# Optimization experiments

Measured on AMD Instinct MI355X. Metric: run time of the kernel, lower is better.

Reference implementation:

```python
import jax, jax.numpy as jnp
from jax import lax
import numpy as np

P = 16          # patch_len
EPS = 1e-5      # BatchNorm eps


def _dct_mats(L):
    # torch_dct DCT-II: ortho matrix Co and scale d s.t. dct(norm=None)(x) = (x @ Co.T) * d,
    # dct(norm='ortho')(x) = x @ Co.T, idct(norm=None)(y) = (y / d) @ Co
    n = jnp.arange(L, dtype=jnp.float32)
    base = jnp.cos(jnp.pi * (2.0 * n[None, :] + 1.0) * n[:, None] / (2.0 * L))
    ck = jnp.where(n == 0, 1.0 / jnp.sqrt(jnp.float32(L)), jnp.sqrt(2.0 / L))
    Co = base * ck[:, None]
    d = jnp.where(n == 0, 2.0 * jnp.sqrt(jnp.float32(L)), jnp.sqrt(2.0 * L))
    return Co, d


def _gelu(t):
    return jax.nn.gelu(t, approximate=False)  # torch nn.GELU default (erf)


def _dw(t, w, pad):  # depthwise Conv1d, t [B,D,L], w [D,k], SAME-style padding
    return lax.conv_general_dilated(t, w[:, None, :], (1,), [(pad, pad)],
                                    feature_group_count=t.shape[1],
                                    dimension_numbers=('NCH', 'OIH', 'NCH'))


def _forward(x, conv1_w, conv1_b, conv2_w, conv2_b, conv3_w, conv3_b,
             dn_g, dn_b, dn_m, dn_v, pn_g, pn_b, pn_m, pn_v,
             embed_w, embed_b, lin_res_w, lin_res_b,
             depth_res_w, depth_res_b, depth_conv_w, depth_conv_b,
             threshold, att_dw_w, att_dw_b, att_conv_w, att_conv_b,
             att_g, att_b, att_m, att_v, fc1_w, fc1_b, fc2_w, fc2_b):
    B, L, D = x.shape
    N = L // P                       # patch_num (stride == patch_len)
    Co, dvec = _dct_mats(L)

    conv1 = lambda t: t * conv1_w[:, None] + conv1_b[:, None]   # grouped 1x1 Conv1d
    bnD = lambda t: (t - dn_m[:, None]) * (dn_g[:, None] / jnp.sqrt(dn_v[:, None] + EPS)) + dn_b[:, None]

    xt = jnp.transpose(x, (0, 2, 1))                 # [B,D,L]
    freq_res = conv1(xt)
    z_dct = (xt @ Co.T) * dvec                       # dct(norm=None)

    # adaptive high-frequency mask
    energy = jnp.sum(z_dct * z_dct, axis=-1)         # [B,D]
    med = jnp.median(energy, axis=1, keepdims=True)
    ne = energy / (med + 1e-6)
    thr = lax.stop_gradient(jnp.quantile(ne, jnp.clip(threshold[0], 0.0, 1.0)))
    mask = (ne > thr).astype(x.dtype)[..., None]     # rows of dominant vars -> 1
    z = _gelu(conv1(z_dct * mask))
    z1 = (z / dvec) @ Co + freq_res                  # idct(norm=None) + residual

    # patching (stride == patch_len -> unfold is a reshape)
    z_p = xt.reshape(B * D, N, P) @ embed_w + embed_b            # [BD,N,P*P]
    z_res = (z_p.reshape(B, D, -1) @ lin_res_w + lin_res_b).transpose(0, 2, 1)  # [B,pred,D]
    time_res = z_p @ depth_res_w + depth_res_b                   # [BD,N,P]
    # depth_conv: grouped Conv1d kernel=stride=P over d_model=P*P
    z_depth = jnp.einsum('bnpj,nj->bnp', z_p.reshape(B * D, N, P, P), depth_conv_w) \
              + depth_conv_b[None, :, None] + time_res
    z_depth = (z_depth - pn_m[:, None]) * (pn_g[:, None] / jnp.sqrt(pn_v[:, None] + EPS)) + pn_b[:, None]
    z2 = _gelu(z_depth).reshape(B, D, L)

    z2_f = conv1(bnD(_gelu((z2 @ Co.T) * dvec)))

    z_r = jax.nn.sigmoid(conv1(bnD(_gelu(_dw(z1, conv2_w, 2) + conv2_b[:, None]))))
    zg = _gelu(z2_f * z_r)

    z1b = _gelu(bnD(_dw(z1, conv3_w, 3) + conv3_b[:, None]))
    z1c = bnD(zg) + z1b

    # DctAtt on z1c * z2: ortho DCT, take 5 low-freq comps per var
    xa = (z1c * z2) @ Co.T                            # [B,D,L]
    low = xa[:, :, :5].reshape(B, D, 5)               # concat layout matches torch loop
    zd = jnp.einsum('bdj,j->bd', low, att_dw_w) + att_dw_b[0]   # Conv1d(1,1,5,stride=5)
    zd = _gelu(zd)
    zd = (zd - att_m[0]) * (att_g[0] / jnp.sqrt(att_v[0] + EPS)) + att_b[0]  # BN(1)
    zd = zd * att_conv_w[0] + att_conv_b[0]           # Conv1d(1,1,1)
    att1 = jax.nn.softmax(zd, axis=-1)[..., None]     # [B,D,1]

    zf = z1c * att1 + z2 * (1.0 - att1)
    out = _gelu(zf @ fc1_w + fc1_b) @ fc2_w + fc2_b   # Mlp -> [B,D,pred]
    return z_res + out.transpose(0, 2, 1)             # [B,pred,D]


def setup_inputs() -> dict:
    key = jax.random.key(0)
    ks = iter(jax.random.split(key, 48))
    B, L, D, pred = 32, 512, 321, 96
    N, dm = L // P, P * P
    r = lambda shape, s=1.0: jax.random.normal(next(ks), shape, jnp.float32) * s
    return dict(
        x=r((B, L, D)),
        conv1_w=r((D,), 0.5) + 1.0, conv1_b=r((D,), 0.1),
        conv2_w=r((D, 5), 0.3), conv2_b=r((D,), 0.1),
        conv3_w=r((D, 7), 0.3), conv3_b=r((D,), 0.1),
        dn_g=jnp.ones((D,), jnp.float32), dn_b=jnp.zeros((D,), jnp.float32),
        dn_m=r((D,), 0.1), dn_v=jnp.ones((D,), jnp.float32),
        pn_g=jnp.ones((N,), jnp.float32), pn_b=jnp.zeros((N,), jnp.float32),
        pn_m=r((N,), 0.1), pn_v=jnp.ones((N,), jnp.float32),
        embed_w=r((P, dm), 0.25), embed_b=r((dm,), 0.02),
        lin_res_w=r((N * dm, pred), 0.01), lin_res_b=r((pred,), 0.02),
        depth_res_w=r((dm, P), 0.06), depth_res_b=r((P,), 0.02),
        depth_conv_w=r((N, P), 0.25), depth_conv_b=r((N,), 0.02),
        threshold=jax.random.uniform(next(ks), (1,), jnp.float32) * 0.5,
        att_dw_w=r((5,), 0.4), att_dw_b=r((1,), 0.1),
        att_conv_w=r((1,)), att_conv_b=r((1,), 0.1),
        att_g=jnp.ones((1,), jnp.float32), att_b=jnp.zeros((1,), jnp.float32),
        att_m=jnp.zeros((1,), jnp.float32), att_v=jnp.ones((1,), jnp.float32),
        fc1_w=r((L, pred), 0.04), fc1_b=r((pred,), 0.02),
        fc2_w=r((pred, pred), 0.1), fc2_b=r((pred,), 0.02),
    )


def reference(x, conv1_w, conv1_b, conv2_w, conv2_b, conv3_w, conv3_b,
              dn_g, dn_b, dn_m, dn_v, pn_g, pn_b, pn_m, pn_v,
              embed_w, embed_b, lin_res_w, lin_res_b,
              depth_res_w, depth_res_b, depth_conv_w, depth_conv_b,
              threshold, att_dw_w, att_dw_b, att_conv_w, att_conv_b,
              att_g, att_b, att_m, att_v, fc1_w, fc1_b, fc2_w, fc2_b):
    return _forward(x, conv1_w, conv1_b, conv2_w, conv2_b, conv3_w, conv3_b,
                    dn_g, dn_b, dn_m, dn_v, pn_g, pn_b, pn_m, pn_v,
                    embed_w, embed_b, lin_res_w, lin_res_b,
                    depth_res_w, depth_res_b, depth_conv_w, depth_conv_b,
                    threshold, att_dw_w, att_dw_b, att_conv_w, att_conv_b,
                    att_g, att_b, att_m, att_v, fc1_w, fc1_b, fc2_w, fc2_b)
```

## Files before the change

kernel.cpp:

```cpp
#include <hip/hip_runtime.h>
#include <cmath>


#define BB   32
#define LL   512
#define DD   321
#define PRED 96
#define M_ROWS (BB*DD)

__device__ __forceinline__ float gelu_f(float x){
  return 0.5f*x*(1.0f + erff(x*0.70710678118654752440f));
}
__device__ __forceinline__ float sigmoid_f(float x){
  return 1.0f/(1.0f+expf(-x));
}

constexpr size_t OFF_COE  = 0;
constexpr size_t OFF_COO  = OFF_COE  + 256*256;
constexpr size_t OFF_COET = OFF_COO  + 256*256;
constexpr size_t OFF_COOT = OFF_COET + 256*256;
constexpr size_t OFF_DVEC = OFF_COOT + 256*256;
constexpr size_t OFF_CATT = OFF_DVEC + 512;
constexpr size_t OFF_FC1T = OFF_CATT + 512;
constexpr size_t OFF_WEFFT= OFF_FC1T + 96*512;
constexpr size_t OFF_CRES = OFF_WEFFT+ 96*512;
constexpr size_t OFF_MP   = OFF_CRES + 128;
constexpr size_t OFF_C2P  = OFF_MP   + 32*256;
constexpr size_t OFF_AF   = OFF_C2P  + 512;
constexpr size_t OFF_CF   = OFF_AF   + 384;
constexpr size_t OFF_DNS  = OFF_CF   + 384;
constexpr size_t OFF_BF   = OFF_DNS  + 384;
constexpr size_t OFF_EN   = OFF_BF   + 384;
constexpr size_t OFF_NE   = OFF_EN   + 10368;
constexpr size_t OFF_THR  = OFF_NE   + 10368;
constexpr size_t OFF_ZDP  = OFF_THR  + 64;
constexpr size_t OFF_ATT1 = OFF_ZDP  + 10368;
constexpr size_t OFF_XT   = OFF_ATT1 + 10368;
constexpr size_t OFF_ZDCT = OFF_XT   + (size_t)M_ROWS*512;
constexpr size_t OFF_Z1   = OFF_ZDCT + (size_t)M_ROWS*512;
constexpr size_t OFF_Z2   = OFF_Z1   + (size_t)M_ROWS*512;
constexpr size_t OFF_Z1C  = OFF_Z2   + (size_t)M_ROWS*512;
constexpr size_t OFF_H    = OFF_Z1C  + (size_t)M_ROWS*512;
constexpr size_t OFF_ZRES = OFF_H    + (size_t)M_ROWS*96;
constexpr size_t OFF_WPART= OFF_ZRES + (size_t)M_ROWS*96;
constexpr size_t OFF_PCRES= OFF_WPART+ 4*96*512;
constexpr size_t WS_FLOATS= OFF_PCRES+ 128*96;

__global__ __launch_bounds__(256)
void k0_dctF(float* __restrict__ CoE, float* __restrict__ CoO,
             float* __restrict__ CoET, float* __restrict__ CoOT,
             float* __restrict__ dvec, float* __restrict__ catt,
             const float* __restrict__ attw)
{
  const float PI_F = 3.14159265358979323846f;
  const float ck0 = 1.0f/sqrtf(512.0f), ckn = sqrtf(2.0f/512.0f);
  int c = blockIdx.x;
  int t = threadIdx.x;
  {
    float a1 = PI_F * (float)(2*t+1);
    float ckE = (c==0) ? ck0 : ckn;
    float aE = a1 * (float)(2*c);
    float aO = a1 * (float)(2*c+1);
    CoE[c*256+t] = cosf(aE * (1.0f/1024.0f)) * ckE;
    CoO[c*256+t] = cosf(aO * (1.0f/1024.0f)) * ckn;
  }
  {
    float a1 = PI_F * (float)(2*c+1);
    float ckE = (t==0) ? ck0 : ckn;
    float aE = a1 * (float)(2*t);
    float aO = a1 * (float)(2*t+1);
    CoET[c*256+t] = cosf(aE * (1.0f/1024.0f)) * ckE;
    CoOT[c*256+t] = cosf(aO * (1.0f/1024.0f)) * ckn;
  }
  if (t==0){
    dvec[2*c]   = (c==0) ? 2.0f*sqrtf(512.0f) : sqrtf(2.0f*512.0f);
    dvec[2*c+1] = sqrtf(2.0f*512.0f);
  }
  if (c==0){
    for (int l=t; l<512; l+=256){
      float sacc=0.f;
      for (int j=0;j<5;j++){
        float ckj = (j==0)? ck0 : ckn;
        float a1 = PI_F*(float)(2*l+1);
        float a2 = a1*(float)j;
        sacc += cosf(a2 * (1.0f/1024.0f))*ckj*attw[j];
      }
      catt[l]=sacc;
    }
  }
}

__global__ __launch_bounds__(256)
void kA_weff(const float* __restrict__ ew_g, const float* __restrict__ eb_g,
             const float* __restrict__ lrw,
             float* __restrict__ Wpart, float* __restrict__ pcres)
{
  const int n = blockIdx.x, kb4 = blockIdx.y;
  __shared__ float ews[16][68];
  __shared__ float ebs[64];
  __shared__ float lw[64][96];
  const int tid = threadIdx.x;
  const int jbase = kb4*64;
  for (int i=tid; i<1024; i+=256){
    int p2 = i>>6, j2 = i&63;
    ews[p2][j2] = ew_g[p2*256 + jbase + j2];
  }
  if (tid < 64) ebs[tid] = eb_g[jbase + tid];
  for (int i=tid; i<1536; i+=256){
    int jj = i/24, c4 = i%24;
    *(float4*)&lw[jj][c4*4] =
      *(const float4*)&lrw[((size_t)(n*256 + jbase + jj))*96 + c4*4];
  }
  __syncthreads();
  const int p = tid>>4, tx = tid&15;
  float acc[6]={0,0,0,0,0,0};
  float accB[6]={0,0,0,0,0,0};
  for (int jj=0; jj<64; jj++){
    float a = ews[p][jj];
    #pragma unroll
    for (int g=0; g<6; g++) acc[g] = fmaf(a, lw[jj][tx+16*g], acc[g]);
    if (p==0){
      float bv = ebs[jj];
      #pragma unroll
      for (int g=0; g<6; g++) accB[g] = fmaf(bv, lw[jj][tx+16*g], accB[g]);
    }
  }
  #pragma unroll
  for (int g=0; g<6; g++){
    int pr = tx + 16*g;
    Wpart[((size_t)kb4*96 + pr)*512 + n*16 + p] = acc[g];
    if (p==0) pcres[(n*4+kb4)*96 + pr] = accB[g];
  }
}

__global__ __launch_bounds__(256)
void kA_fin(const float* __restrict__ Wpart, const float* __restrict__ pcres,
            const float* __restrict__ lrb,
            float* __restrict__ WeffT, float* __restrict__ cres)
{
  int b = blockIdx.x;
  if (b < 192){
    int i = b*256 + threadIdx.x;
    WeffT[i] = (Wpart[i] + Wpart[49152+i]) + (Wpart[2*49152+i] + Wpart[3*49152+i]);
  } else {
    int pr = threadIdx.x;
    if (pr < 96){
      float s = lrb[pr];
      for (int nn=0; nn<128; nn++) s += pcres[nn*96+pr];
      cres[pr] = s;
    }
  }
}

__global__ __launch_bounds__(256)
void kT_fc1(const float* __restrict__ fc1_w, float* __restrict__ fc1T)
{
  __shared__ float t[32][33];
  int c0 = blockIdx.x*32;
  int l0 = blockIdx.y*32;
  int tid=threadIdx.x; int j=tid&31, i0=tid>>5;
  for (int ii=0; ii<32; ii+=8){
    int l=l0+i0+ii, c=c0+j;
    t[i0+ii][j] = (c<96)? fc1_w[l*96+c] : 0.f;
  }
  __syncthreads();
  for (int ii=0; ii<32; ii+=8){
    int c=c0+i0+ii, l=l0+j;
    if (c<96) fc1T[(size_t)c*512 + l] = t[j][i0+ii];
  }
}

__global__ __launch_bounds__(256)
void k0_depth(const float* __restrict__ embed_w, const float* __restrict__ embed_b,
              const float* __restrict__ drw, const float* __restrict__ drb,
              const float* __restrict__ dcw, const float* __restrict__ dcb,
              const float* __restrict__ png, const float* __restrict__ pnb,
              const float* __restrict__ pnm, const float* __restrict__ pnv,
              float* __restrict__ Mp, float* __restrict__ c2p)
{
  int n = blockIdx.x; int tid = threadIdx.x;
  int q = tid>>4, p = tid&15;
  float acc = 0.f;
  for (int j=0;j<16;j++)  acc = fmaf(embed_w[q*256 + p*16 + j], dcw[n*16+j], acc);
  float wtr = 0.f;
  for (int j=0;j<256;j++) wtr = fmaf(embed_w[q*256 + j], drw[j*16+p], wtr);
  float sn = png[n]/sqrtf(pnv[n]+1e-5f);
  Mp[n*256 + q*16 + p] = (acc + wtr) * sn;
  if (q==0){
    float c = dcb[n];
    for (int j=0;j<16;j++)  c = fmaf(embed_b[p*16+j], dcw[n*16+j], c);
    float ctr = drb[p];
    for (int j=0;j<256;j++) ctr = fmaf(embed_b[j], drw[j*16+p], ctr);
    c += ctr;
    c2p[n*16+p] = (c - pnm[n])*sn + pnb[n];
  }
}

__global__ void k0_fold(const float* __restrict__ w1, const float* __restrict__ b1,
                        const float* __restrict__ g,  const float* __restrict__ bbq,
                        const float* __restrict__ mq, const float* __restrict__ vq,
                        float* __restrict__ Af, float* __restrict__ Cf,
                        float* __restrict__ dns, float* __restrict__ Bf)
{
  int d = blockIdx.x*256 + threadIdx.x;
  if (d >= DD) return;
  float s  = g[d]/sqrtf(vq[d]+1e-5f);
  float bf = bbq[d] - mq[d]*s;
  dns[d]=s; Bf[d]=bf; Af[d]=s*w1[d]; Cf[d]=bf*w1[d]+b1[d];
}

__global__ __launch_bounds__(256)
void k1_transpose(const float* __restrict__ x, float* __restrict__ xt)
{
  int b = blockIdx.z; int l0 = blockIdx.y*32; int d0 = blockIdx.x*32;
  __shared__ float t[32][33];
  int tid=threadIdx.x; int j = tid&31, i0 = tid>>5;
  for (int ii=0; ii<32; ii+=8){
    int l = l0 + i0+ii; int d = d0 + j;
    t[i0+ii][j] = (d<DD) ? x[((size_t)b*512 + l)*DD + d] : 0.f;
  }
  __syncthreads();
  for (int ii=0; ii<32; ii+=8){
    int d = d0 + i0+ii; int l = l0 + j;
    if (d<DD) xt[((size_t)b*DD+d)*512 + l] = t[j][i0+ii];
  }
}

template<int OP>
__global__ __launch_bounds__(256)
void gemm_dual(const float* __restrict__ A, const float* __restrict__ BE,
               const float* __restrict__ BO, float* __restrict__ C, int M,
               const float* __restrict__ p0, const float* __restrict__ p1,
               const float* __restrict__ p2, const float* __restrict__ p3)
{
  __shared__ float Ae[32][132];
  __shared__ float Ao[32][132];
  __shared__ float Be[32][68];
  __shared__ float Bo[32][68];
  const int tid = threadIdx.x;
  const int tx = tid & 15, ty = tid >> 4;
  const int rb = blockIdx.y * 128, cb = blockIdx.x * 64;

  float accE[8][4], accO[8][4];
  #pragma unroll
  for (int i=0;i<8;i++)
    #pragma unroll
    for (int j=0;j<4;j++){ accE[i][j]=0.f; accO[i][j]=0.f; }

  for (int kb=0; kb<256; kb+=32){
    if constexpr (OP==0 || OP==2){
      #pragma unroll
      for (int i=0;i<4;i++){
        int idx = tid + i*256;
        int row = idx >> 3, k4 = (idx & 7)*4;
        int r = rb + row;
        float4 lo = make_float4(0.f,0.f,0.f,0.f);
        float4 hi = make_float4(0.f,0.f,0.f,0.f);
        if (r < M){
          lo = *(const float4*)(A + (size_t)r*512 + kb + k4);
          hi = *(const float4*)(A + (size_t)r*512 + (508 - kb - k4));
        }
        Ae[k4+0][row] = lo.x + hi.w;  Ao[k4+0][row] = lo.x - hi.w;
        Ae[k4+1][row] = lo.y + hi.z;  Ao[k4+1][row] = lo.y - hi.z;
        Ae[k4+2][row] = lo.z + hi.y;  Ao[k4+2][row] = lo.z - hi.y;
        Ae[k4+3][row] = lo.w + hi.x;  Ao[k4+3][row] = lo.w - hi.x;
      }
    } else {
      #pragma unroll
      for (int i=0;i<8;i++){
        int idx = tid + i*256;
        int row = idx >> 4, c0 = (idx & 15)*4;
        int r = rb + row;
        float4 v = make_float4(0.f,0.f,0.f,0.f);
        if (r < M) v = *(const float4*)(A + (size_t)r*512 + 2*kb + c0);
        int kk = c0 >> 1;
        Ae[kk+0][row] = v.x;  Ao[kk+0][row] = v.y;
        Ae[kk+1][row] = v.z;  Ao[kk+1][row] = v.w;
      }
    }
    #pragma unroll
    for (int i=0;i<2;i++){
      int idx = tid + i*256;
      int crow = idx >> 3, k4 = (idx & 7)*4;
      int c = cb + crow;
      float4 ve = *(const float4*)(BE + (size_t)c*256 + kb + k4);
      float4 vo = *(const float4*)(BO + (size_t)c*256 + kb + k4);
      Be[k4+0][crow]=ve.x; Be[k4+1][crow]=ve.y; Be[k4+2][crow]=ve.z; Be[k4+3][crow]=ve.w;
      Bo[k4+0][crow]=vo.x; Bo[k4+1][crow]=vo.y; Bo[k4+2][crow]=vo.z; Bo[k4+3][crow]=vo.w;
    }
    __syncthreads();
    #pragma unroll
    for (int kk=0; kk<32; kk++){
      const float4 ae0 = *(const float4*)&Ae[kk][ty*8];
      const float4 ae1 = *(const float4*)&Ae[kk][ty*8+4];
      const float4 ao0 = *(const float4*)&Ao[kk][ty*8];
      const float4 ao1 = *(const float4*)&Ao[kk][ty*8+4];
      const float4 be  = *(const float4*)&Be[kk][tx*4];
      const float4 bo  = *(const float4*)&Bo[kk][tx*4];
      float aev[8]={ae0.x,ae0.y,ae0.z,ae0.w,ae1.x,ae1.y,ae1.z,ae1.w};
      float aov[8]={ao0.x,ao0.y,ao0.z,ao0.w,ao1.x,ao1.y,ao1.z,ao1.w};
      float bev[4]={be.x,be.y,be.z,be.w};
      float bov[4]={bo.x,bo.y,bo.z,bo.w};
      #pragma unroll
      for (int i=0;i<8;i++)
        #pragma unroll
        for (int j=0;j<4;j++){
          accE[i][j]=fmaf(aev[i],bev[j],accE[i][j]);
          accO[i][j]=fmaf(aov[i],bov[j],accO[i][j]);
        }
    }
    __syncthreads();
  }

  const int c0 = cb + tx*4;
  #pragma unroll
  for (int i=0;i<8;i++){
    const int r = rb + ty*8 + i;
    if (r >= M) continue;
    if constexpr (OP==0){
      float4 o0 = make_float4(accE[i][0]*p0[2*c0+0], accO[i][0]*p0[2*c0+1],
                              accE[i][1]*p0[2*c0+2], accO[i][1]*p0[2*c0+3]);
      float4 o1 = make_float4(accE[i][2]*p0[2*c0+4], accO[i][2]*p0[2*c0+5],
                              accE[i][3]*p0[2*c0+6], accO[i][3]*p0[2*c0+7]);
      *(float4*)(C + (size_t)r*512 + 2*c0)     = o0;
      *(float4*)(C + (size_t)r*512 + 2*c0 + 4) = o1;
    } else if constexpr (OP==2){
      int d = r % DD;
      float w = p0[d], bo = p1[d];
      float4 o0 = make_float4(gelu_f(accE[i][0]*p3[2*c0+0])*w+bo,
                              gelu_f(accO[i][0]*p3[2*c0+1])*w+bo,
                              gelu_f(accE[i][1]*p3[2*c0+2])*w+bo,
                              gelu_f(accO[i][1]*p3[2*c0+3])*w+bo);
      float4 o1 = make_float4(gelu_f(accE[i][2]*p3[2*c0+4])*w+bo,
                              gelu_f(accO[i][2]*p3[2*c0+5])*w+bo,
                              gelu_f(accE[i][3]*p3[2*c0+6])*w+bo,
                              gelu_f(accO[i][3]*p3[2*c0+7])*w+bo);
      *(float4*)(C + (size_t)r*512 + 2*c0)     = o0;
      *(float4*)(C + (size_t)r*512 + 2*c0 + 4) = o1;
    } else {
      int d = r % DD;
      float w = p0[d], bo = p1[d];
      float4 xf = *(const float4*)(p2 + (size_t)r*512 + c0);
      float4 xr = *(const float4*)(p2 + (size_t)r*512 + 508 - c0);
      float4 of, orv;
      of.x = accE[i][0]+accO[i][0] + xf.x*w+bo;
      of.y = accE[i][1]+accO[i][1] + xf.y*w+bo;
      of.z = accE[i][2]+accO[i][2] + xf.z*w+bo;
      of.w = accE[i][3]+accO[i][3] + xf.w*w+bo;
      orv.x = accE[i][3]-accO[i][3] + xr.x*w+bo;
      orv.y = accE[i][2]-accO[i][2] + xr.y*w+bo;
      orv.z = accE[i][1]-accO[i][1] + xr.z*w+bo;
      orv.w = accE[i][0]-accO[i][0] + xr.w*w+bo;
      *(float4*)(C + (size_t)r*512 + c0)       = of;
      *(float4*)(C + (size_t)r*512 + 508 - c0) = orv;
    }
  }
}

template<int OP>
__global__ __launch_bounds__(256)
void gemm_nt(const float* __restrict__ A, const float* __restrict__ B,
             float* __restrict__ C, int M, int Ncols, int ldc,
             const float* __restrict__ p0)
{
  __shared__ float As[32][132];
  __shared__ float Bs[32][68];
  const int tid = threadIdx.x;
  const int tx = tid & 15, ty = tid >> 4;
  const int rb = blockIdx.y * 128, cb = blockIdx.x * 64;

  float acc[8][4];
  #pragma unroll
  for (int i=0;i<8;i++)
    #pragma unroll
    for (int j=0;j<4;j++) acc[i][j]=0.f;

  for (int kb=0; kb<512; kb+=32){
    #pragma unroll
    for (int i=0;i<4;i++){
      int idx = tid + i*256;
      int row = idx >> 3, k4 = (idx & 7)*4;
      float4 v = make_float4(0.f,0.f,0.f,0.f);
      int r = rb + row;
      if (r < M) v = *reinterpret_cast<const float4*>(A + (size_t)r*512 + kb + k4);
      As[k4+0][row]=v.x; As[k4+1][row]=v.y; As[k4+2][row]=v.z; As[k4+3][row]=v.w;
    }
    #pragma unroll
    for (int i=0;i<2;i++){
      int idx = tid + i*256;
      int row = idx >> 3, k4 = (idx & 7)*4;
      float4 v = make_float4(0.f,0.f,0.f,0.f);
      int c = cb + row;
      if (c < Ncols) v = *reinterpret_cast<const float4*>(B + (size_t)c*512 + kb + k4);
      Bs[k4+0][row]=v.x; Bs[k4+1][row]=v.y; Bs[k4+2][row]=v.z; Bs[k4+3][row]=v.w;
    }
    __syncthreads();
    #pragma unroll
    for (int kk=0; kk<32; kk++){
      const float4 a0 = *reinterpret_cast<const float4*>(&As[kk][ty*8]);
      const float4 a1 = *reinterpret_cast<const float4*>(&As[kk][ty*8+4]);
      const float4 b0 = *reinterpret_cast<const float4*>(&Bs[kk][tx*4]);
      float av[8]={a0.x,a0.y,a0.z,a0.w,a1.x,a1.y,a1.z,a1.w};
      float bv[4]={b0.x,b0.y,b0.z,b0.w};
      #pragma unroll
      for (int i=0;i<8;i++)
        #pragma unroll
        for (int j=0;j<4;j++) acc[i][j]=fmaf(av[i],bv[j],acc[i][j]);
    }
    __syncthreads();
  }

  #pragma unroll
  for (int i=0;i<8;i++){
    const int r = rb + ty*8 + i;
    if (r >= M) continue;
    #pragma unroll
    for (int j=0;j<4;j++){
      int c = cb + tx*4 + j;
      if (c < Ncols){
        if constexpr (OP==3) C[(size_t)r*ldc + c] = gelu_f(acc[i][j] + p0[c]);
        else                 C[(size_t)r*ldc + c] = acc[i][j] + p0[c];
      }
    }
  }
}

__global__ __launch_bounds__(256)
void k_energy(const float* __restrict__ zdct, float* __restrict__ energy)
{
  int r=blockIdx.x, tid=threadIdx.x;
  __shared__ float rbuf[256];
  float acc=0.f;
  for (int k=tid;k<512;k+=256){ float v=zdct[(size_t)r*512+k]; acc=fmaf(v,v,acc); }
  rbuf[tid]=acc; __syncthreads();
  for (int st=128;st>0;st>>=1){ if(tid<st) rbuf[tid]+=rbuf[tid+st]; __syncthreads(); }
  if (tid==0) energy[r]=rbuf[0];
}

__global__ __launch_bounds__(256)
void k3_median(const float* __restrict__ energy, float* __restrict__ ne)
{
  int b = blockIdx.x, tid=threadIdx.x;
  __shared__ float e[DD];
  __shared__ float medv;
  for (int i=tid;i<DD;i+=256) e[i]=energy[b*DD+i];
  __syncthreads();
  for (int i=tid;i<DD;i+=256){
    float v=e[i]; int lt=0, eq=0;
    for (int j=0;j<DD;j++){ float u=e[j]; lt += (u<v); eq += (u==v); }
    if (lt<=160 && 160<lt+eq) medv=v;
  }
  __syncthreads();
  float den = medv + 1e-6f;
  for (int i=tid;i<DD;i+=256) ne[b*DD+i] = e[i]/den;
}

__global__ __launch_bounds__(1024)
void k3_thr(const float* __restrict__ ne, const float* __restrict__ thrin,
            float* __restrict__ out)
{
  __shared__ int hist[256];
  __shared__ unsigned sPrefix; __shared__ int sRank;
  int tid = threadIdx.x;
  float q = fminf(fmaxf(thrin[0],0.f),1.f);
  float pos = q * (float)(M_ROWS-1);
  int lo = (int)floorf(pos); int hi = (int)ceilf(pos);
  float frac = pos - floorf(pos);
  float vals[2];
  for (int s=0;s<2;s++){
    int rank = s ? hi : lo;
    unsigned prefix=0, pmask=0;
    for (int pass=0; pass<4; pass++){
      int shift = 24 - 8*pass;
      if (tid<256) hist[tid]=0;
      __syncthreads();
      for (int i=tid;i<M_ROWS;i+=1024){
        unsigned u = __float_as_uint(ne[i]);
        if ((u & pmask)==prefix) atomicAdd(&hist[(u>>shift)&255u],1);
      }
      __syncthreads();
      if (tid==0){
        int cum=0;
        for (int bkt=0;bkt<256;bkt++){
          int c=hist[bkt];
          if (cum + c > rank){ sPrefix = prefix | ((unsigned)bkt<<(unsigned)shift); sRank = rank - cum; break; }
          cum += c;
        }
      }
      __syncthreads();
      prefix = sPrefix; rank = sRank; pmask |= (0xFFu<<(unsigned)shift);
      __syncthreads();
    }
    vals[s] = __uint_as_float(prefix);
  }
  if (tid==0) out[0] = vals[0]*(1.0f-frac) + vals[1]*frac;
}

__global__ void k4_pre(float* __restrict__ zdct, const float* __restrict__ ne,
                       const float* __restrict__ thr, const float* __restrict__ w1,
                       const float* __restrict__ b1, const float* __restrict__ dvec)
{
  size_t idx = (size_t)blockIdx.x*256 + threadIdx.x;
  int r = (int)(idx>>7);
  int k0 = ((int)idx & 127)*4;
  float m  = (ne[r] > thr[0]) ? 1.f : 0.f;
  int d = r % DD;
  float w = w1[d]*m, bo = b1[d];
  float4 v = ((float4*)zdct)[idx];
  v.x = gelu_f(fmaf(v.x,w,bo))/dvec[k0+0];
  v.y = gelu_f(fmaf(v.y,w,bo))/dvec[k0+1];
  v.z = gelu_f(fmaf(v.z,w,bo))/dvec[k0+2];
  v.w = gelu_f(fmaf(v.w,w,bo))/dvec[k0+3];
  ((float4*)zdct)[idx]=v;
}

__global__ __launch_bounds__(256)
void k5_z2(const float* __restrict__ xt, const float* __restrict__ Mp,
           const float* __restrict__ c2p, float* __restrict__ z2)
{
  int r = blockIdx.x, tid=threadIdx.x;
  __shared__ float row[512];
  for (int i=tid;i<512;i+=256) row[i]=xt[(size_t)r*512+i];
  __syncthreads();
  for (int idx=tid; idx<512; idx+=256){
    int n = idx>>4, p = idx&15;
    float acc = c2p[idx];
    const float* Mn = Mp + n*256 + p;
    #pragma unroll
    for (int qq=0;qq<16;qq++) acc = fmaf(row[n*16+qq], Mn[qq*16], acc);
    z2[(size_t)r*512+idx] = gelu_f(acc);
  }
}

__global__ __launch_bounds__(256)
void k7_fuse(const float* __restrict__ z1, const float* __restrict__ z2f,
             const float* __restrict__ z2, float* __restrict__ z1c,
             float* __restrict__ zdpre,
             const float* __restrict__ c2w, const float* __restrict__ c2b,
             const float* __restrict__ c3w, const float* __restrict__ c3b,
             const float* __restrict__ Af,  const float* __restrict__ Cf,
             const float* __restrict__ dns, const float* __restrict__ Bf,
             const float* __restrict__ catt)
{
  int r = blockIdx.x, tid=threadIdx.x;
  int d = r % DD;
  __shared__ float zrow[518];
  __shared__ float rbuf[256];
  for (int i=tid;i<518;i+=256){
    int l = i-3;
    zrow[i] = (l>=0 && l<512) ? z1[(size_t)r*512+l] : 0.f;
  }
  __syncthreads();
  float w2[5], w3[7];
  #pragma unroll
  for (int t=0;t<5;t++) w2[t]=c2w[d*5+t];
  #pragma unroll
  for (int t=0;t<7;t++) w3[t]=c3w[d*7+t];
  const float cb2=c2b[d], cb3=c3b[d];
  const float af=Af[d], cf=Cf[d], s=dns[d], bf=Bf[d];
  float dotacc=0.f;
  for (int l=tid;l<512;l+=256){
    float c5=cb2;
    #pragma unroll
    for (int t=0;t<5;t++) c5 = fmaf(zrow[l+t+1], w2[t], c5);
    float zr  = sigmoid_f(fmaf(gelu_f(c5),af,cf));
    float zgv = gelu_f(z2f[(size_t)r*512+l]*zr);
    float c7=cb3;
    #pragma unroll
    for (int t=0;t<7;t++) c7 = fmaf(zrow[l+t], w3[t], c7);
    float z1b = gelu_f(fmaf(c7,s,bf));
    float v = fmaf(zgv,s,bf) + z1b;
    z1c[(size_t)r*512+l]=v;
    dotacc = fmaf(v*z2[(size_t)r*512+l], catt[l], dotacc);
  }
  rbuf[tid]=dotacc; __syncthreads();
  for (int st=128;st>0;st>>=1){ if(tid<st) rbuf[tid]+=rbuf[tid+st]; __syncthreads(); }
  if (tid==0) zdpre[r]=rbuf[0];
}

__global__ __launch_bounds__(256)
void k8_att(const float* __restrict__ zdpre, float* __restrict__ att1,
            const float* __restrict__ adwb, const float* __restrict__ acw,
            const float* __restrict__ acb,  const float* __restrict__ ag,
            const float* __restrict__ ab,   const float* __restrict__ am,
            const float* __restrict__ av)
{
  int b=blockIdx.x, t=threadIdx.x;
  __shared__ float sred[256];
  float vloc[2];
  float mx=-INFINITY;
  float sA = ag[0]/sqrtf(av[0]+1e-5f);
  #pragma unroll
  for (int ii=0;ii<2;ii++){
    int d=t+ii*256;
    float v=-INFINITY;
    if (d<DD){
      float zd = zdpre[b*DD+d] + adwb[0];
      zd = gelu_f(zd);
      zd = (zd-am[0])*sA + ab[0];
      zd = zd*acw[0] + acb[0];
      v=zd;
    }
    vloc[ii]=v; mx=fmaxf(mx,v);
  }
  sred[t]=mx; __syncthreads();
  for (int st=128;st>0;st>>=1){ if (t<st) sred[t]=fmaxf(sred[t],sred[t+st]); __syncthreads(); }
  float m=sred[0]; __syncthreads();
  float e0 = (t<DD)     ? expf(vloc[0]-m) : 0.f;
  float e1 = (t+256<DD) ? expf(vloc[1]-m) : 0.f;
  sred[t]=e0+e1; __syncthreads();
  for (int st=128;st>0;st>>=1){ if (t<st) sred[t]+=sred[t+st]; __syncthreads(); }
  float sum=sred[0];
  if (t<DD)     att1[b*DD+t]     = e0/sum;
  if (t+256<DD) att1[b*DD+t+256] = e1/sum;
}

__global__ void k8b_zf(const float* __restrict__ z1c, const float* __restrict__ z2,
                       const float* __restrict__ att1, float* __restrict__ zf)
{
  size_t idx = (size_t)blockIdx.x*256 + threadIdx.x;
  int r = (int)(idx>>7);
  float a = att1[r];
  float4 v1 = ((const float4*)z1c)[idx];
  float4 v2 = ((const float4*)z2)[idx];
  float4 o;
  o.x = v1.x*a + v2.x*(1.f-a);
  o.y = v1.y*a + v2.y*(1.f-a);
  o.z = v1.z*a + v2.z*(1.f-a);
  o.w = v1.w*a + v2.w*(1.f-a);
  ((float4*)zf)[idx]=o;
}

__global__ __launch_bounds__(256)
void k9_final(const float* __restrict__ h, const float* __restrict__ zres,
              const float* __restrict__ fc2_w, const float* __restrict__ fc2_b,
              float* __restrict__ outF)
{
  int b = blockIdx.y; int d0 = blockIdx.x*32;
  __shared__ float f2[96*96];
  __shared__ float hs[32][97];
  __shared__ float zs[32][97];
  int tid=threadIdx.x;
  for (int i=tid;i<96*96;i+=256) f2[i]=fc2_w[i];
  for (int i=tid;i<32*96;i+=256){
    int dl = i/96, p = i%96; int d = d0+dl;
    float hv=0.f, zv=0.f;
    if (d<DD){ hv = h[((size_t)b*DD+d)*96+p]; zv = zres[((size_t)b*DD+d)*96+p]; }
    hs[dl][p]=hv; zs[dl][p]=zv;
  }
  __syncthreads();
  int tx = tid & 31, ty = tid >> 5;
  int d = d0+tx;
  float acc[12];
  #pragma unroll
  for (int kc=0;kc<12;kc++) acc[kc]=0.f;
  for (int p=0;p<96;p++){
    float hv = hs[tx][p];
    #pragma unroll
    for (int kc=0;kc<12;kc++) acc[kc] = fmaf(hv, f2[p*96 + ty + kc*8], acc[kc]);
  }
  if (d<DD){
    #pragma unroll
    for (int kc=0;kc<12;kc++){
      int c = ty + kc*8;
      outF[((size_t)b*96 + c)*DD + d] = acc[kc] + fc2_b[c] + zs[tx][c];
    }
  }
}

extern "C" void kernel_launch(void* const* d_in, const int* in_sizes, int n_in,
                              void* d_out, int out_size, void* d_ws, size_t ws_size,
                              hipStream_t stream)
{
  (void)in_sizes; (void)n_in; (void)out_size; (void)ws_size;
  const float* x        =(const float*)d_in[0];
  const float* conv1_w  =(const float*)d_in[1];
  const float* conv1_b  =(const float*)d_in[2];
  const float* conv2_w  =(const float*)d_in[3];
  const float* conv2_b  =(const float*)d_in[4];
  const float* conv3_w  =(const float*)d_in[5];
  const float* conv3_b  =(const float*)d_in[6];
  const float* dn_g     =(const float*)d_in[7];
  const float* dn_b     =(const float*)d_in[8];
  const float* dn_m     =(const float*)d_in[9];
  const float* dn_v     =(const float*)d_in[10];
  const float* pn_g     =(const float*)d_in[11];
  const float* pn_b     =(const float*)d_in[12];
  const float* pn_m     =(const float*)d_in[13];
  const float* pn_v     =(const float*)d_in[14];
  const float* embed_w  =(const float*)d_in[15];
  const float* embed_b  =(const float*)d_in[16];
  const float* lin_res_w=(const float*)d_in[17];
  const float* lin_res_b=(const float*)d_in[18];
  const float* depth_res_w=(const float*)d_in[19];
  const float* depth_res_b=(const float*)d_in[20];
  const float* depth_conv_w=(const float*)d_in[21];
  const float* depth_conv_b=(const float*)d_in[22];
  const float* threshold=(const float*)d_in[23];
  const float* att_dw_w =(const float*)d_in[24];
  const float* att_dw_b =(const float*)d_in[25];
  const float* att_conv_w=(const float*)d_in[26];
  const float* att_conv_b=(const float*)d_in[27];
  const float* att_g    =(const float*)d_in[28];
  const float* att_b    =(const float*)d_in[29];
  const float* att_m    =(const float*)d_in[30];
  const float* att_v    =(const float*)d_in[31];
  const float* fc1_w    =(const float*)d_in[32];
  const float* fc1_b    =(const float*)d_in[33];
  const float* fc2_w    =(const float*)d_in[34];
  const float* fc2_b    =(const float*)d_in[35];

  float* ws   = (float*)d_ws;
  float* CoE  = ws + OFF_COE;
  float* CoO  = ws + OFF_COO;
  float* CoET = ws + OFF_COET;
  float* CoOT = ws + OFF_COOT;
  float* dvec = ws + OFF_DVEC;
  float* catt = ws + OFF_CATT;
  float* fc1T = ws + OFF_FC1T;
  float* WeffT= ws + OFF_WEFFT;
  float* cres = ws + OFF_CRES;
  float* Mp   = ws + OFF_MP;
  float* c2p  = ws + OFF_C2P;
  float* Af   = ws + OFF_AF;
  float* Cf   = ws + OFF_CF;
  float* dns  = ws + OFF_DNS;
  float* Bf   = ws + OFF_BF;
  float* energy=ws + OFF_EN;
  float* ne   = ws + OFF_NE;
  float* thr  = ws + OFF_THR;
  float* zdpre= ws + OFF_ZDP;
  float* att1 = ws + OFF_ATT1;
  float* xt   = ws + OFF_XT;
  float* zdct = ws + OFF_ZDCT;
  float* z1   = ws + OFF_Z1;
  float* z2   = ws + OFF_Z2;
  float* z1c  = ws + OFF_Z1C;
  float* h    = ws + OFF_H;
  float* zres = ws + OFF_ZRES;
  float* Wpart= ws + OFF_WPART;
  float* pcres= ws + OFF_PCRES;

  k0_dctF <<<256, 256, 0, stream>>>(CoE, CoO, CoET, CoOT, dvec, catt, att_dw_w);
  kA_weff <<<dim3(32,4), 256, 0, stream>>>(embed_w, embed_b, lin_res_w, Wpart, pcres);
  kA_fin  <<<193, 256, 0, stream>>>(Wpart, pcres, lin_res_b, WeffT, cres);
  kT_fc1  <<<dim3(3,16), 256, 0, stream>>>(fc1_w, fc1T);
  k0_depth<<<32, 256, 0, stream>>>(embed_w, embed_b, depth_res_w, depth_res_b,
                                   depth_conv_w, depth_conv_b, pn_g, pn_b, pn_m, pn_v,
                                   Mp, c2p);
  k0_fold <<<2, 256, 0, stream>>>(conv1_w, conv1_b, dn_g, dn_b, dn_m, dn_v,
                                  Af, Cf, dns, Bf);

  k1_transpose<<<dim3(11,16,BB), 256, 0, stream>>>(x, xt);
  gemm_dual<0><<<dim3(4,81), 256, 0, stream>>>(xt, CoE, CoO, zdct, M_ROWS,
                                               dvec, nullptr, nullptr, nullptr);
  k_energy <<<M_ROWS, 256, 0, stream>>>(zdct, energy);
  k3_median<<<BB, 256, 0, stream>>>(energy, ne);
  k3_thr   <<<1, 1024, 0, stream>>>(ne, threshold, thr);

  k4_pre   <<<5136, 256, 0, stream>>>(zdct, ne, thr, conv1_w, conv1_b, dvec);
  gemm_dual<1><<<dim3(4,81), 256, 0, stream>>>(zdct, CoET, CoOT, z1, M_ROWS,
                                               conv1_w, conv1_b, xt, nullptr);

  k5_z2    <<<M_ROWS, 256, 0, stream>>>(xt, Mp, c2p, z2);
  gemm_dual<2><<<dim3(4,81), 256, 0, stream>>>(z2, CoE, CoO, zdct, M_ROWS,
                                               Af, Cf, nullptr, dvec);

  k7_fuse  <<<M_ROWS, 256, 0, stream>>>(z1, zdct, z2, z1c, zdpre,
                                        conv2_w, conv2_b, conv3_w, conv3_b,
                                        Af, Cf, dns, Bf, catt);
  k8_att   <<<BB, 256, 0, stream>>>(zdpre, att1, att_dw_b, att_conv_w, att_conv_b,
                                    att_g, att_b, att_m, att_v);
  k8b_zf   <<<5136, 256, 0, stream>>>(z1c, z2, att1, z1);

  gemm_nt<3><<<dim3(2,81), 256, 0, stream>>>(z1, fc1T, h, M_ROWS, 96, 96, fc1_b);
  gemm_nt<4><<<dim3(2,81), 256, 0, stream>>>(xt, WeffT, zres, M_ROWS, 96, 96, cres);
  k9_final <<<dim3(11,BB), 256, 0, stream>>>(h, zres, fc2_w, fc2_b, (float*)d_out);
}
```

Before: 767.0 us.

## Shrink DCT GEMM tiles, fuse attention blend into merged fc1/residual GEMM

The dual-DCT GEMM moves to 64x32 tiles with 128-thread blocks, which raises the block count to fill more compute units, and its dvec scale factors become compile-time constants. The separate attention-blend kernel is removed, and the blend of z1c and z2 is folded into the A-tile load of the fc1 GEMM. The two 96-column GEMMs are merged into one launch that uses blockIdx.z to pick fc1 or the residual weight. This removes a full elementwise pass over a large buffer and two launches, at the cost of smaller tiles with less register reuse per thread.

```diff
diff --git a/kernel.cpp b/kernel.cpp
--- a/kernel.cpp
+++ b/kernel.cpp
@@ -227,23 +227,24 @@
 }
 
 template<int OP>
-__global__ __launch_bounds__(256)
+__global__ __launch_bounds__(128, 4)
 void gemm_dual(const float* __restrict__ A, const float* __restrict__ BE,
                const float* __restrict__ BO, float* __restrict__ C, int M,
                const float* __restrict__ p0, const float* __restrict__ p1,
-               const float* __restrict__ p2, const float* __restrict__ p3)
-{
-  __shared__ float Ae[32][132];
-  __shared__ float Ao[32][132];
-  __shared__ float Be[32][68];
-  __shared__ float Bo[32][68];
+               const float* __restrict__ p2)
+{
+  __shared__ float Ae[32][68];
+  __shared__ float Ao[32][68];
+  __shared__ float Be[32][36];
+  __shared__ float Bo[32][36];
   const int tid = threadIdx.x;
-  const int tx = tid & 15, ty = tid >> 4;
-  const int rb = blockIdx.y * 128, cb = blockIdx.x * 64;
-
-  float accE[8][4], accO[8][4];
-  #pragma unroll
-  for (int i=0;i<8;i++)
+  const int tx = tid & 7, ty = tid >> 3;
+  const int rb = blockIdx.y * 64, cb = blockIdx.x * 32;
+  const float dv0 = 45.25483399593904f, dvn = 32.0f;
+
+  float accE[4][4], accO[4][4];
+  #pragma unroll
+  for (int i=0;i<4;i++)
     #pragma unroll
     for (int j=0;j<4;j++){ accE[i][j]=0.f; accO[i][j]=0.f; }
 
@@ -251,7 +252,7 @@
     if constexpr (OP==0 || OP==2){
       #pragma unroll
       for (int i=0;i<4;i++){
-        int idx = tid + i*256;
+        int idx = tid + i*128;
         int row = idx >> 3, k4 = (idx & 7)*4;
         int r = rb + row;
         float4 lo = make_float4(0.f,0.f,0.f,0.f);
@@ -268,7 +269,7 @@
     } else {
       #pragma unroll
       for (int i=0;i<8;i++){
-        int idx = tid + i*256;
+        int idx = tid + i*128;
         int row = idx >> 4, c0 = (idx & 15)*4;
         int r = rb + row;
         float4 v = make_float4(0.f,0.f,0.f,0.f);
@@ -280,7 +281,7 @@
     }
     #pragma unroll
     for (int i=0;i<2;i++){
-      int idx = tid + i*256;
+      int idx = tid + i*128;
       int crow = idx >> 3, k4 = (idx & 7)*4;
       int c = cb + crow;
       float4 ve = *(const float4*)(BE + (size_t)c*256 + kb + k4);
@@ -291,18 +292,16 @@
     __syncthreads();
     #pragma unroll
     for (int kk=0; kk<32; kk++){
-      const float4 ae0 = *(const float4*)&Ae[kk][ty*8];
-      const float4 ae1 = *(const float4*)&Ae[kk][ty*8+4];
-      const float4 ao0 = *(const float4*)&Ao[kk][ty*8];
-      const float4 ao1 = *(const float4*)&Ao[kk][ty*8+4];
-      const float4 be  = *(const float4*)&Be[kk][tx*4];
-      const float4 bo  = *(const float4*)&Bo[kk][tx*4];
-      float aev[8]={ae0.x,ae0.y,ae0.z,ae0.w,ae1.x,ae1.y,ae1.z,ae1.w};
-      float aov[8]={ao0.x,ao0.y,ao0.z,ao0.w,ao1.x,ao1.y,ao1.z,ao1.w};
+      const float4 ae = *(const float4*)&Ae[kk][ty*4];
+      const float4 ao = *(const float4*)&Ao[kk][ty*4];
+      const float4 be = *(const float4*)&Be[kk][tx*4];
+      const float4 bo = *(const float4*)&Bo[kk][tx*4];
+      float aev[4]={ae.x,ae.y,ae.z,ae.w};
+      float aov[4]={ao.x,ao.y,ao.z,ao.w};
       float bev[4]={be.x,be.y,be.z,be.w};
       float bov[4]={bo.x,bo.y,bo.z,bo.w};
       #pragma unroll
-      for (int i=0;i<8;i++)
+      for (int i=0;i<4;i++)
         #pragma unroll
         for (int j=0;j<4;j++){
           accE[i][j]=fmaf(aev[i],bev[j],accE[i][j]);
@@ -314,27 +313,29 @@
 
   const int c0 = cb + tx*4;
   #pragma unroll
-  for (int i=0;i<8;i++){
-    const int r = rb + ty*8 + i;
+  for (int i=0;i<4;i++){
+    const int r = rb + ty*4 + i;
     if (r >= M) continue;
     if constexpr (OP==0){
-      float4 o0 = make_float4(accE[i][0]*p0[2*c0+0], accO[i][0]*p0[2*c0+1],
-                              accE[i][1]*p0[2*c0+2], accO[i][1]*p0[2*c0+3]);
-      float4 o1 = make_float4(accE[i][2]*p0[2*c0+4], accO[i][2]*p0[2*c0+5],
-                              accE[i][3]*p0[2*c0+6], accO[i][3]*p0[2*c0+7]);
+      float d0e = (c0==0) ? dv0 : dvn;
+      float4 o0 = make_float4(accE[i][0]*d0e, accO[i][0]*dvn,
+                              accE[i][1]*dvn, accO[i][1]*dvn);
+      float4 o1 = make_float4(accE[i][2]*dvn, accO[i][2]*dvn,
+                              accE[i][3]*dvn, accO[i][3]*dvn);
       *(float4*)(C + (size_t)r*512 + 2*c0)     = o0;
       *(float4*)(C + (size_t)r*512 + 2*c0 + 4) = o1;
     } else if constexpr (OP==2){
       int d = r % DD;
       float w = p0[d], bo = p1[d];
-      float4 o0 = make_float4(gelu_f(accE[i][0]*p3[2*c0+0])*w+bo,
-                              gelu_f(accO[i][0]*p3[2*c0+1])*w+bo,
-                              gelu_f(accE[i][1]*p3[2*c0+2])*w+bo,
-                              gelu_f(accO[i][1]*p3[2*c0+3])*w+bo);
-      float4 o1 = make_float4(gelu_f(accE[i][2]*p3[2*c0+4])*w+bo,
-                              gelu_f(accO[i][2]*p3[2*c0+5])*w+bo,
-                              gelu_f(accE[i][3]*p3[2*c0+6])*w+bo,
-                              gelu_f(accO[i][3]*p3[2*c0+7])*w+bo);
+      float d0e = (c0==0) ? dv0 : dvn;
+      float4 o0 = make_float4(gelu_f(accE[i][0]*d0e)*w+bo,
+                              gelu_f(accO[i][0]*dvn)*w+bo,
+                              gelu_f(accE[i][1]*dvn)*w+bo,
+                              gelu_f(accO[i][1]*dvn)*w+bo);
+      float4 o1 = make_float4(gelu_f(accE[i][2]*dvn)*w+bo,
+                              gelu_f(accO[i][2]*dvn)*w+bo,
+                              gelu_f(accE[i][3]*dvn)*w+bo,
+                              gelu_f(accO[i][3]*dvn)*w+bo);
       *(float4*)(C + (size_t)r*512 + 2*c0)     = o0;
       *(float4*)(C + (size_t)r*512 + 2*c0 + 4) = o1;
     } else {
@@ -357,17 +358,27 @@
   }
 }
 
-template<int OP>
-__global__ __launch_bounds__(256)
-void gemm_nt(const float* __restrict__ A, const float* __restrict__ B,
-             float* __restrict__ C, int M, int Ncols, int ldc,
-             const float* __restrict__ p0)
-{
-  __shared__ float As[32][132];
+__global__ __launch_bounds__(128, 4)
+void gemm96(const float* __restrict__ z1c, const float* __restrict__ z2,
+            const float* __restrict__ att1, const float* __restrict__ xt,
+            const float* __restrict__ fc1T, const float* __restrict__ WeffT,
+            float* __restrict__ h, float* __restrict__ zres,
+            const float* __restrict__ fc1_b, const float* __restrict__ cres, int M)
+{
+  __shared__ float As[32][68];
   __shared__ float Bs[32][68];
+  __shared__ float att_s[64];
   const int tid = threadIdx.x;
   const int tx = tid & 15, ty = tid >> 4;
-  const int rb = blockIdx.y * 128, cb = blockIdx.x * 64;
+  const int rb = blockIdx.y * 64, cb = blockIdx.x * 64;
+  const int z = blockIdx.z;
+  const float* Bmat = z ? WeffT : fc1T;
+
+  if (z==0 && tid < 64){
+    int r = rb + tid;
+    att_s[tid] = (r < M) ? att1[r] : 0.f;
+  }
+  __syncthreads();
 
   float acc[8][4];
   #pragma unroll
@@ -378,28 +389,40 @@
   for (int kb=0; kb<512; kb+=32){
     #pragma unroll
     for (int i=0;i<4;i++){
-      int idx = tid + i*256;
+      int idx = tid + i*128;
       int row = idx >> 3, k4 = (idx & 7)*4;
+      int r = rb + row;
       float4 v = make_float4(0.f,0.f,0.f,0.f);
-      int r = rb + row;
-      if (r < M) v = *reinterpret_cast<const float4*>(A + (size_t)r*512 + kb + k4);
+      if (r < M){
+        if (z==0){
+          float4 v1 = *(const float4*)(z1c + (size_t)r*512 + kb + k4);
+          float4 v2 = *(const float4*)(z2  + (size_t)r*512 + kb + k4);
+          float a = att_s[row];
+          v.x = v2.x + a*(v1.x - v2.x);
+          v.y = v2.y + a*(v1.y - v2.y);
+          v.z = v2.z + a*(v1.z - v2.z);
+          v.w = v2.w + a*(v1.w - v2.w);
+        } else {
+          v = *(const float4*)(xt + (size_t)r*512 + kb + k4);
+        }
+      }
       As[k4+0][row]=v.x; As[k4+1][row]=v.y; As[k4+2][row]=v.z; As[k4+3][row]=v.w;
     }
     #pragma unroll
-    for (int i=0;i<2;i++){
-      int idx = tid + i*256;
-      int row = idx >> 3, k4 = (idx & 7)*4;
+    for (int i=0;i<4;i++){
+      int idx = tid + i*128;
+      int crow = idx >> 3, k4 = (idx & 7)*4;
+      int c = cb + crow;
       float4 v = make_float4(0.f,0.f,0.f,0.f);
-      int c = cb + row;
-      if (c < Ncols) v = *reinterpret_cast<const float4*>(B + (size_t)c*512 + kb + k4);
-      Bs[k4+0][row]=v.x; Bs[k4+1][row]=v.y; Bs[k4+2][row]=v.z; Bs[k4+3][row]=v.w;
+      if (c < 96) v = *(const float4*)(Bmat + (size_t)c*512 + kb + k4);
+      Bs[k4+0][crow]=v.x; Bs[k4+1][crow]=v.y; Bs[k4+2][crow]=v.z; Bs[k4+3][crow]=v.w;
     }
     __syncthreads();
     #pragma unroll
     for (int kk=0; kk<32; kk++){
-      const float4 a0 = *reinterpret_cast<const float4*>(&As[kk][ty*8]);
-      const float4 a1 = *reinterpret_cast<const float4*>(&As[kk][ty*8+4]);
-      const float4 b0 = *reinterpret_cast<const float4*>(&Bs[kk][tx*4]);
+      const float4 a0 = *(const float4*)&As[kk][ty*8];
+      const float4 a1 = *(const float4*)&As[kk][ty*8+4];
+      const float4 b0 = *(const float4*)&Bs[kk][tx*4];
       float av[8]={a0.x,a0.y,a0.z,a0.w,a1.x,a1.y,a1.z,a1.w};
       float bv[4]={b0.x,b0.y,b0.z,b0.w};
       #pragma unroll
@@ -417,9 +440,9 @@
     #pragma unroll
     for (int j=0;j<4;j++){
       int c = cb + tx*4 + j;
-      if (c < Ncols){
-        if constexpr (OP==3) C[(size_t)r*ldc + c] = gelu_f(acc[i][j] + p0[c]);
-        else                 C[(size_t)r*ldc + c] = acc[i][j] + p0[c];
+      if (c < 96){
+        if (z==0) h[(size_t)r*96 + c]    = gelu_f(acc[i][j] + fc1_b[c]);
+        else      zres[(size_t)r*96 + c] = acc[i][j] + cres[c];
       }
     }
   }
@@ -613,22 +636,6 @@
   float sum=sred[0];
   if (t<DD)     att1[b*DD+t]     = e0/sum;
   if (t+256<DD) att1[b*DD+t+256] = e1/sum;
-}
-
-__global__ void k8b_zf(const float* __restrict__ z1c, const float* __restrict__ z2,
-                       const float* __restrict__ att1, float* __restrict__ zf)
-{
-  size_t idx = (size_t)blockIdx.x*256 + threadIdx.x;
-  int r = (int)(idx>>7);
-  float a = att1[r];
-  float4 v1 = ((const float4*)z1c)[idx];
-  float4 v2 = ((const float4*)z2)[idx];
-  float4 o;
-  o.x = v1.x*a + v2.x*(1.f-a);
-  o.y = v1.y*a + v2.y*(1.f-a);
-  o.z = v1.z*a + v2.z*(1.f-a);
-  o.w = v1.w*a + v2.w*(1.f-a);
-  ((float4*)zf)[idx]=o;
 }
 
 __global__ __launch_bounds__(256)
@@ -752,28 +759,26 @@
                                   Af, Cf, dns, Bf);
 
   k1_transpose<<<dim3(11,16,BB), 256, 0, stream>>>(x, xt);
-  gemm_dual<0><<<dim3(4,81), 256, 0, stream>>>(xt, CoE, CoO, zdct, M_ROWS,
-                                               dvec, nullptr, nullptr, nullptr);
+  gemm_dual<0><<<dim3(8,161), 128, 0, stream>>>(xt, CoE, CoO, zdct, M_ROWS,
+                                                nullptr, nullptr, nullptr);
   k_energy <<<M_ROWS, 256, 0, stream>>>(zdct, energy);
   k3_median<<<BB, 256, 0, stream>>>(energy, ne);
   k3_thr   <<<1, 1024, 0, stream>>>(ne, threshold, thr);
 
   k4_pre   <<<5136, 256, 0, stream>>>(zdct, ne, thr, conv1_w, conv1_b, dvec);
-  gemm_dual<1><<<dim3(4,81), 256, 0, stream>>>(zdct, CoET, CoOT, z1, M_ROWS,
-                                               conv1_w, conv1_b, xt, nullptr);
-
+  gemm_dual<1><<<dim3(8,161), 128, 0, stream>>>(zdct, CoET, CoOT, z1, M_ROWS,
+                                                conv1_w, conv1_b, xt);
   k5_z2    <<<M_ROWS, 256, 0, stream>>>(xt, Mp, c2p, z2);
-  gemm_dual<2><<<dim3(4,81), 256, 0, stream>>>(z2, CoE, CoO, zdct, M_ROWS,
-                                               Af, Cf, nullptr, dvec);
+  gemm_dual<2><<<dim3(8,161), 128, 0, stream>>>(z2, CoE, CoO, zdct, M_ROWS,
+                                                Af, Cf, nullptr);
 
   k7_fuse  <<<M_ROWS, 256, 0, stream>>>(z1, zdct, z2, z1c, zdpre,
                                         conv2_w, conv2_b, conv3_w, conv3_b,
                                         Af, Cf, dns, Bf, catt);
   k8_att   <<<BB, 256, 0, stream>>>(zdpre, att1, att_dw_b, att_conv_w, att_conv_b,
                                     att_g, att_b, att_m, att_v);
-  k8b_zf   <<<5136, 256, 0, stream>>>(z1c, z2, att1, z1);
-
-  gemm_nt<3><<<dim3(2,81), 256, 0, stream>>>(z1, fc1T, h, M_ROWS, 96, 96, fc1_b);
-  gemm_nt<4><<<dim3(2,81), 256, 0, stream>>>(xt, WeffT, zres, M_ROWS, 96, 96, cres);
+
+  gemm96   <<<dim3(2,161,2), 128, 0, stream>>>(z1c, z2, att1, xt, fc1T, WeffT,
+                                               h, zres, fc1_b, cres, M_ROWS);
   k9_final <<<dim3(11,BB), 256, 0, stream>>>(h, zres, fc2_w, fc2_b, (float*)d_out);
 }
```

New measurement: 723.4 us. -5.7%, faster.
